# Performance work log

Measured on AMD Instinct MI355X. Metric: run time of the kernel, lower is better.

## Reference

```python
import jax, jax.numpy as jnp
import numpy as np

N = 100000
E = 1600000


def gcn_conv(x, W, b, src, dst, n_nodes):
    """PyG GCNConv: linear -> add self loops -> sym-normalized scatter-add."""
    h = x @ W  # [N, out]
    # degree with self-loops: deg[i] = 1 + in_degree(i)
    deg = jax.ops.segment_sum(jnp.ones((src.shape[0],), h.dtype), dst,
                              num_segments=n_nodes) + 1.0
    dinv = jax.lax.rsqrt(deg)  # deg >= 1 always
    norm = dinv[src] * dinv[dst]  # [E]
    # neighbor messages + self-loop contribution (norm = deg^-1)
    agg = jax.ops.segment_sum(h[src] * norm[:, None], dst,
                              num_segments=n_nodes)
    return agg + h * (dinv * dinv)[:, None] + b


def setup_inputs() -> dict:
    key = jax.random.key(0)
    k1, k2, k3, k4 = jax.random.split(key, 4)
    x = jax.random.normal(k1, (N, 128), dtype=jnp.float32)
    edge_index = jax.random.randint(k2, (2, E), 0, N, dtype=jnp.int64)
    W1 = jax.random.normal(k3, (128, 64), dtype=jnp.float32) * (1.0 / np.sqrt(128))
    b1 = jnp.zeros((64,), jnp.float32)
    W2 = jax.random.normal(k4, (64, 40), dtype=jnp.float32) * (1.0 / np.sqrt(64))
    b2 = jnp.zeros((40,), jnp.float32)
    return {"x": x, "edge_index": edge_index, "W1": W1, "b1": b1,
            "W2": W2, "b2": b2}


def reference(x, edge_index, W1, b1, W2, b2):
    src, dst = edge_index[0], edge_index[1]
    h = gcn_conv(x, W1, b1, src, dst, N)
    h = jax.nn.relu(h)
    # dropout is identity in eval mode; mask_features is a no-op
    h = gcn_conv(h, W2, b2, src, dst, N)
    return jax.nn.log_softmax(h, axis=1)
```

## Files before the change

### kernel.cpp

```cpp
#include <hip/hip_runtime.h>
#include <math.h>

#define N_NODES 100000
#define N_EDGES 1600000
#define F_IN    128
#define F_HID   64
#define F_OUT   40

#define BIN_SHIFT 9
#define NBINS     196
#define BIN_CAP   10240
#define FILL_BLOCKS 256

typedef unsigned int  uint;
typedef unsigned short ushort;
typedef __attribute__((ext_vector_type(8))) short bf16x8;
typedef __attribute__((ext_vector_type(4))) float f32x4;

__device__ __forceinline__ unsigned short f2bf(float f) {
    uint u = __float_as_uint(f);
    u = (u + 0x7FFF + ((u >> 16) & 1)) >> 16;
    return (unsigned short)u;
}
__device__ __forceinline__ uint pack2bf(float a, float b) {
    return (uint)f2bf(a) | ((uint)f2bf(b) << 16);
}
__device__ __forceinline__ float bf_lo(uint u) { return __uint_as_float(u << 16); }
__device__ __forceinline__ float bf_hi(uint u) { return __uint_as_float(u & 0xFFFF0000u); }

__global__ void init_kernel(int* __restrict__ bcursor) {
    int t = threadIdx.x;
    if (t < NBINS) bcursor[t] = t * BIN_CAP;
}

__global__ void binfill_kernel(const int* __restrict__ src, const int* __restrict__ dst,
                               int* __restrict__ bcursor, int* __restrict__ bins, int E) {
    __shared__ int lcount[NBINS];
    __shared__ int gbase[NBINS];
    int tid = threadIdx.x;
    for (int i = tid; i < NBINS; i += 256) lcount[i] = 0;
    __syncthreads();
    int chunk = (E + gridDim.x - 1) / gridDim.x;
    int beg = blockIdx.x * chunk, end = min(E, beg + chunk);
    for (int e = beg + tid; e < end; e += 256)
        atomicAdd(&lcount[dst[e] >> BIN_SHIFT], 1);
    __syncthreads();
    for (int i = tid; i < NBINS; i += 256) {
        gbase[i] = lcount[i] ? atomicAdd(&bcursor[i], lcount[i]) : 0;
        lcount[i] = 0;
    }
    __syncthreads();
    for (int e = beg + tid; e < end; e += 256) {
        int d = dst[e];
        int b = d >> BIN_SHIFT;
        int p = atomicAdd(&lcount[b], 1);
        bins[gbase[b] + p] = src[e] | ((d & 511) << 17);
    }
}

__global__ void binsort_kernel(const int* __restrict__ bcursor, const int* __restrict__ bins,
                               int* __restrict__ csr, int* __restrict__ rowstart,
                               int* __restrict__ rowcnt, float* __restrict__ dinv) {
    __shared__ int hist[512];
    __shared__ int scan[512];
    __shared__ int cur[512];
    __shared__ int sorted[BIN_CAP];
    int b = blockIdx.x, t = threadIdx.x;
    int base = b * BIN_CAP;
    int cnt = bcursor[b] - base;
    hist[t] = 0;
    __syncthreads();
    for (int i = t; i < cnt; i += 512)
        atomicAdd(&hist[(unsigned)bins[base + i] >> 17], 1);
    __syncthreads();
    int v = hist[t];
    scan[t] = v;
    __syncthreads();
    for (int off = 1; off < 512; off <<= 1) {
        int u = (t >= off) ? scan[t - off] : 0;
        __syncthreads();
        scan[t] += u;
        __syncthreads();
    }
    int excl = scan[t] - v;
    cur[t] = excl;
    int node = (b << BIN_SHIFT) + t;
    if (node < N_NODES) {
        rowstart[node] = base + excl;
        rowcnt[node]   = v;
        dinv[node] = rsqrtf((float)v + 1.0f);
    }
    __syncthreads();
    for (int i = t; i < cnt; i += 512) {
        int p   = bins[base + i];
        int pos = atomicAdd(&cur[(unsigned)p >> 17], 1);
        sorted[pos] = p & 0x1FFFF;
    }
    __syncthreads();
    for (int i = t; i < cnt; i += 512)
        csr[base + i] = sorted[i];
}

__global__ void wtrans_kernel(const float* __restrict__ W, uint* __restrict__ Wt) {
    int tid = threadIdx.x;
    for (int i = tid; i < 4096; i += 256) {
        int c  = i >> 6;
        int kp = i & 63;
        Wt[i] = pack2bf(W[(2 * kp) * F_HID + c], W[(2 * kp + 1) * F_HID + c]);
    }
}

#define XPITCH 68
__global__ __launch_bounds__(256) void gemm1_kernel(const float* __restrict__ x,
                                                    const uint* __restrict__ Wt,
                                                    ushort* __restrict__ h, int n) {
    __shared__ __align__(16) uint Xu[64 * XPITCH];
    __shared__ __align__(16) uint Wu[64 * XPITCH];
    int tid = threadIdx.x;
    int node0 = blockIdx.x * 64;

    {
        int c = tid >> 2, qq = tid & 3;
        const uint4* gsrc = (const uint4*)&Wt[c * 64 + qq * 16];
        uint4* ldst = (uint4*)&Wu[c * XPITCH + qq * 16];
        #pragma unroll
        for (int j = 0; j < 4; ++j) ldst[j] = gsrc[j];
    }
    {
        int row = tid >> 2, qq = tid & 3;
        int node = node0 + row;
        uint4* ldst = (uint4*)&Xu[row * XPITCH + qq * 16];
        if (node < n) {
            const float4* gsrc = (const float4*)&x[(size_t)node * F_IN + qq * 32];
            #pragma unroll
            for (int j = 0; j < 4; ++j) {
                float4 a = gsrc[2 * j], b = gsrc[2 * j + 1];
                uint4 o;
                o.x = pack2bf(a.x, a.y); o.y = pack2bf(a.z, a.w);
                o.z = pack2bf(b.x, b.y); o.w = pack2bf(b.z, b.w);
                ldst[j] = o;
            }
        } else {
            uint4 z = make_uint4(0, 0, 0, 0);
            #pragma unroll
            for (int j = 0; j < 4; ++j) ldst[j] = z;
        }
    }
    __syncthreads();

    int wv   = tid >> 6;
    int lane = tid & 63;
    int lrow = lane & 15;
    int quad = lane >> 4;

    bf16x8 bfrag[4][4];
    #pragma unroll
    for (int t = 0; t < 4; ++t)
        #pragma unroll
        for (int s = 0; s < 4; ++s)
            bfrag[t][s] = *(const bf16x8*)&Wu[(t * 16 + lrow) * XPITCH + s * 16 + quad * 4];

    f32x4 acc[4];
    #pragma unroll
    for (int t = 0; t < 4; ++t) acc[t] = (f32x4){0.f, 0.f, 0.f, 0.f};

    #pragma unroll
    for (int s = 0; s < 4; ++s) {
        bf16x8 afrag = *(const bf16x8*)&Xu[(wv * 16 + lrow) * XPITCH + s * 16 + quad * 4];
        #pragma unroll
        for (int t = 0; t < 4; ++t)
            acc[t] = __builtin_amdgcn_mfma_f32_16x16x32_bf16(afrag, bfrag[t][s], acc[t], 0, 0, 0);
    }

    #pragma unroll
    for (int t = 0; t < 4; ++t) {
        #pragma unroll
        for (int i = 0; i < 4; ++i) {
            int node = node0 + wv * 16 + quad * 4 + i;
            if (node < n) h[(size_t)node * F_HID + t * 16 + lrow] = f2bf(acc[t][i]);
        }
    }
}

__global__ void agg1_kernel(const int* __restrict__ rowstart, const int* __restrict__ rowcnt,
                            const int* __restrict__ csr, const float* __restrict__ dinv,
                            const ushort* __restrict__ h, const float* __restrict__ b,
                            ushort* __restrict__ out, int n) {
    int wv   = threadIdx.x >> 6;
    int lane = threadIdx.x & 63;
    int slot = lane >> 3;
    int c    = lane & 7;
    int node0 = blockIdx.x * 16 + wv * 4;
    for (int nn = 0; nn < 4; ++nn) {
        int node = node0 + nn;
        if (node >= n) break;
        int beg = rowstart[node], end = beg + rowcnt[node];
        float acc[8] = {0.f,0.f,0.f,0.f,0.f,0.f,0.f,0.f};
        for (int base = beg; base < end; base += 64) {
            int idx = base + lane;
            int   sid = 0; float wgt = 0.f;
            if (idx < end) { sid = csr[idx]; wgt = dinv[sid]; }
            int cnt    = min(64, end - base);
            int groups = (cnt + 7) >> 3;
            int g = 0;
            for (; g + 2 <= groups; g += 2) {
                int   sA = __shfl(sid, g * 8 + slot);
                float wA = __shfl(wgt, g * 8 + slot);
                int   sB = __shfl(sid, g * 8 + 8 + slot);
                float wB = __shfl(wgt, g * 8 + 8 + slot);
                uint4 hA = *(const uint4*)&h[(size_t)sA * F_HID + (c << 3)];
                uint4 hB = *(const uint4*)&h[(size_t)sB * F_HID + (c << 3)];
                acc[0] += bf_lo(hA.x) * wA; acc[1] += bf_hi(hA.x) * wA;
                acc[2] += bf_lo(hA.y) * wA; acc[3] += bf_hi(hA.y) * wA;
                acc[4] += bf_lo(hA.z) * wA; acc[5] += bf_hi(hA.z) * wA;
                acc[6] += bf_lo(hA.w) * wA; acc[7] += bf_hi(hA.w) * wA;
                acc[0] += bf_lo(hB.x) * wB; acc[1] += bf_hi(hB.x) * wB;
                acc[2] += bf_lo(hB.y) * wB; acc[3] += bf_hi(hB.y) * wB;
                acc[4] += bf_lo(hB.z) * wB; acc[5] += bf_hi(hB.z) * wB;
                acc[6] += bf_lo(hB.w) * wB; acc[7] += bf_hi(hB.w) * wB;
            }
            if (g < groups) {
                int   sA = __shfl(sid, g * 8 + slot);
                float wA = __shfl(wgt, g * 8 + slot);
                uint4 hA = *(const uint4*)&h[(size_t)sA * F_HID + (c << 3)];
                acc[0] += bf_lo(hA.x) * wA; acc[1] += bf_hi(hA.x) * wA;
                acc[2] += bf_lo(hA.y) * wA; acc[3] += bf_hi(hA.y) * wA;
                acc[4] += bf_lo(hA.z) * wA; acc[5] += bf_hi(hA.z) * wA;
                acc[6] += bf_lo(hA.w) * wA; acc[7] += bf_hi(hA.w) * wA;
            }
        }
        #pragma unroll
        for (int m = 8; m < 64; m <<= 1) {
            #pragma unroll
            for (int k = 0; k < 8; ++k) acc[k] += __shfl_xor(acc[k], m);
        }
        if (slot == 0) {
            float di = dinv[node];
            uint4 hs = *(const uint4*)&h[(size_t)node * F_HID + (c << 3)];
            float self[8] = { bf_lo(hs.x), bf_hi(hs.x), bf_lo(hs.y), bf_hi(hs.y),
                              bf_lo(hs.z), bf_hi(hs.z), bf_lo(hs.w), bf_hi(hs.w) };
            float4 b0 = *(const float4*)&b[c << 3];
            float4 b1v = *(const float4*)&b[(c << 3) + 4];
            float bb[8] = { b0.x, b0.y, b0.z, b0.w, b1v.x, b1v.y, b1v.z, b1v.w };
            ushort o[8];
            #pragma unroll
            for (int k = 0; k < 8; ++k) {
                float v = fmaxf(acc[k] * di + self[k] * di * di + bb[k], 0.f);
                o[k] = f2bf(v);
            }
            uint4 pk;
            pk.x = (uint)o[0] | ((uint)o[1] << 16);
            pk.y = (uint)o[2] | ((uint)o[3] << 16);
            pk.z = (uint)o[4] | ((uint)o[5] << 16);
            pk.w = (uint)o[6] | ((uint)o[7] << 16);
            *(uint4*)&out[(size_t)node * F_HID + (c << 3)] = pk;
        }
    }
}

__global__ void gemm2_kernel(const ushort* __restrict__ a, const float* __restrict__ W,
                             ushort* __restrict__ h, int n) {
    __shared__ float Wl[F_HID * F_OUT];
    int tid = threadIdx.x;
    for (int i = tid; i < F_HID * F_OUT; i += 256) Wl[i] = W[i];
    __syncthreads();
    long long idx = (long long)blockIdx.x * 256 + tid;
    if (idx >= (long long)n * F_OUT) return;
    int node = (int)(idx / F_OUT);
    int col  = (int)(idx - (long long)node * F_OUT);
    const uint* arow = (const uint*)(a + (size_t)node * F_HID);
    float acc = 0.0f;
    #pragma unroll 8
    for (int k = 0; k < F_HID / 2; ++k) {
        uint u = arow[k];
        acc += bf_lo(u) * Wl[(2 * k) * F_OUT + col] + bf_hi(u) * Wl[(2 * k + 1) * F_OUT + col];
    }
    h[idx] = f2bf(acc);
}

__global__ void agg2_kernel(const int* __restrict__ rowstart, const int* __restrict__ rowcnt,
                            const int* __restrict__ csr, const float* __restrict__ dinv,
                            const ushort* __restrict__ h, const float* __restrict__ b,
                            float* __restrict__ out, int n) {
    int wv   = threadIdx.x >> 6;
    int lane = threadIdx.x & 63;
    int slot = lane / 5;
    int c    = lane - slot * 5;
    int node0 = blockIdx.x * 16 + wv * 4;
    float bb[8];
    if (lane < 5) {
        float4 b0 = *(const float4*)&b[lane * 8];
        float4 b1 = *(const float4*)&b[lane * 8 + 4];
        bb[0] = b0.x; bb[1] = b0.y; bb[2] = b0.z; bb[3] = b0.w;
        bb[4] = b1.x; bb[5] = b1.y; bb[6] = b1.z; bb[7] = b1.w;
    }
    for (int nn = 0; nn < 4; ++nn) {
        int node = node0 + nn;
        if (node >= n) break;
        int beg = rowstart[node], end = beg + rowcnt[node];
        float acc[8] = {0.f,0.f,0.f,0.f,0.f,0.f,0.f,0.f};
        for (int base = beg; base < end; base += 60) {
            int idx = base + lane;
            int   sid = 0; float wgt = 0.f;
            if (lane < 60 && idx < end) { sid = csr[idx]; wgt = dinv[sid]; }
            int cnt    = min(60, end - base);
            int groups = (cnt + 11) / 12;
            int g = 0;
            for (; g + 2 <= groups; g += 2) {
                int   slA = (slot < 12) ? (g * 12 + slot) : 60;
                int   slB = (slot < 12) ? (g * 12 + 12 + slot) : 60;
                int   sA = __shfl(sid, slA);
                float wA = __shfl(wgt, slA);
                int   sB = __shfl(sid, slB);
                float wB = __shfl(wgt, slB);
                uint4 hA = *(const uint4*)&h[(size_t)sA * F_OUT + c * 8];
                uint4 hB = *(const uint4*)&h[(size_t)sB * F_OUT + c * 8];
                acc[0] += bf_lo(hA.x) * wA; acc[1] += bf_hi(hA.x) * wA;
                acc[2] += bf_lo(hA.y) * wA; acc[3] += bf_hi(hA.y) * wA;
                acc[4] += bf_lo(hA.z) * wA; acc[5] += bf_hi(hA.z) * wA;
                acc[6] += bf_lo(hA.w) * wA; acc[7] += bf_hi(hA.w) * wA;
                acc[0] += bf_lo(hB.x) * wB; acc[1] += bf_hi(hB.x) * wB;
                acc[2] += bf_lo(hB.y) * wB; acc[3] += bf_hi(hB.y) * wB;
                acc[4] += bf_lo(hB.z) * wB; acc[5] += bf_hi(hB.z) * wB;
                acc[6] += bf_lo(hB.w) * wB; acc[7] += bf_hi(hB.w) * wB;
            }
            if (g < groups) {
                int   slA = (slot < 12) ? (g * 12 + slot) : 60;
                int   sA = __shfl(sid, slA);
                float wA = __shfl(wgt, slA);
                uint4 hA = *(const uint4*)&h[(size_t)sA * F_OUT + c * 8];
                acc[0] += bf_lo(hA.x) * wA; acc[1] += bf_hi(hA.x) * wA;
                acc[2] += bf_lo(hA.y) * wA; acc[3] += bf_hi(hA.y) * wA;
                acc[4] += bf_lo(hA.z) * wA; acc[5] += bf_hi(hA.z) * wA;
                acc[6] += bf_lo(hA.w) * wA; acc[7] += bf_hi(hA.w) * wA;
            }
        }
        float r[8];
        #pragma unroll
        for (int k = 0; k < 8; ++k) {
            float t6 = __shfl(acc[k], lane + 30);
            float s6 = acc[k] + t6;
            float t3 = __shfl(s6, lane + 15);
            float s3 = s6 + t3;
            float t1 = __shfl(s3, lane + 5);
            float t2 = __shfl(s3, lane + 10);
            r[k] = s3 + t1 + t2;
        }
        float val[8];
        float m = -INFINITY;
        if (lane < 5) {
            float di = dinv[node];
            uint4 hs = *(const uint4*)&h[(size_t)node * F_OUT + lane * 8];
            float self[8] = { bf_lo(hs.x), bf_hi(hs.x), bf_lo(hs.y), bf_hi(hs.y),
                              bf_lo(hs.z), bf_hi(hs.z), bf_lo(hs.w), bf_hi(hs.w) };
            #pragma unroll
            for (int k = 0; k < 8; ++k) {
                val[k] = r[k] * di + self[k] * di * di + bb[k];
                m = fmaxf(m, val[k]);
            }
        }
        #pragma unroll
        for (int off = 1; off < 8; off <<= 1) m = fmaxf(m, __shfl_xor(m, off));
        float p = 0.f;
        if (lane < 5) {
            #pragma unroll
            for (int k = 0; k < 8; ++k) p += __expf(val[k] - m);
        }
        #pragma unroll
        for (int off = 1; off < 8; off <<= 1) p += __shfl_xor(p, off);
        float lse = m + __logf(p);
        if (lane < 5) {
            float4 o0, o1;
            o0.x = val[0] - lse; o0.y = val[1] - lse; o0.z = val[2] - lse; o0.w = val[3] - lse;
            o1.x = val[4] - lse; o1.y = val[5] - lse; o1.z = val[6] - lse; o1.w = val[7] - lse;
            *(float4*)&out[(size_t)node * F_OUT + lane * 8]     = o0;
            *(float4*)&out[(size_t)node * F_OUT + lane * 8 + 4] = o1;
        }
    }
}

extern "C" void kernel_launch(void* const* d_in, const int* in_sizes, int n_in,
                              void* d_out, int out_size, void* d_ws, size_t ws_size,
                              hipStream_t stream) {
    const float* x  = (const float*)d_in[0];
    const int*   ei = (const int*)d_in[1];
    const float* W1 = (const float*)d_in[2];
    const float* b1 = (const float*)d_in[3];
    const float* W2 = (const float*)d_in[4];
    const float* b2 = (const float*)d_in[5];
    const int* src = ei;
    const int* dst = ei + N_EDGES;

    char* p = (char*)d_ws;
    int*    bcursor  = (int*)p;     p += (size_t)(NBINS + 4) * 4;
    int*    bins     = (int*)p;     p += (size_t)NBINS * BIN_CAP * 4;
    int*    csr_src  = (int*)p;     p += (size_t)NBINS * BIN_CAP * 4;
    int*    rowstart = (int*)p;     p += (size_t)(N_NODES + 4) * 4;
    int*    rowcnt   = (int*)p;     p += (size_t)(N_NODES + 4) * 4;
    float*  dinv     = (float*)p;   p += (size_t)N_NODES * 4;
    uint*   Wtb      = (uint*)p;    p += (size_t)4096 * 4;
    ushort* h1b      = (ushort*)p;  p += (size_t)N_NODES * F_HID * 2;
    ushort* out1b    = (ushort*)p;  p += (size_t)N_NODES * F_HID * 2;
    ushort* h2b      = (ushort*)p;  p += (size_t)N_NODES * F_OUT * 2;
    float*  out      = (float*)d_out;

    init_kernel   <<<1, 256, 0, stream>>>(bcursor);
    binfill_kernel<<<FILL_BLOCKS, 256, 0, stream>>>(src, dst, bcursor, bins, N_EDGES);
    binsort_kernel<<<NBINS, 512, 0, stream>>>(bcursor, bins, csr_src, rowstart, rowcnt, dinv);
    wtrans_kernel <<<1, 256, 0, stream>>>(W1, Wtb);
    gemm1_kernel  <<<(N_NODES + 63) / 64, 256, 0, stream>>>(x, Wtb, h1b, N_NODES);
    agg1_kernel   <<<(N_NODES + 15) / 16, 256, 0, stream>>>(rowstart, rowcnt, csr_src, dinv,
                                                            h1b, b1, out1b, N_NODES);
    gemm2_kernel  <<<((N_NODES * F_OUT) + 255) / 256, 256, 0, stream>>>(out1b, W2, h2b, N_NODES);
    agg2_kernel   <<<(N_NODES + 15) / 16, 256, 0, stream>>>(rowstart, rowcnt, csr_src, dinv,
                                                            h2b, b2, out, N_NODES);
}
```

Baseline: 303.0 us.

## Halve bin size, fuse prep kernels, one node per wavefront in aggregation

```diff
diff --git a/kernel.cpp b/kernel.cpp
--- a/kernel.cpp
+++ b/kernel.cpp
@@ -7,10 +7,10 @@
 #define F_HID   64
 #define F_OUT   40
 
-#define BIN_SHIFT 9
-#define NBINS     196
-#define BIN_CAP   10240
-#define FILL_BLOCKS 256
+#define BIN_SHIFT 8
+#define NBINS     392
+#define BIN_CAP   5120
+#define FILL_BLOCKS 512
 
 typedef unsigned int  uint;
 typedef unsigned short ushort;
@@ -28,9 +28,15 @@
 __device__ __forceinline__ float bf_lo(uint u) { return __uint_as_float(u << 16); }
 __device__ __forceinline__ float bf_hi(uint u) { return __uint_as_float(u & 0xFFFF0000u); }
 
-__global__ void init_kernel(int* __restrict__ bcursor) {
-    int t = threadIdx.x;
-    if (t < NBINS) bcursor[t] = t * BIN_CAP;
+__global__ void prep_kernel(const float* __restrict__ W, uint* __restrict__ Wt,
+                            int* __restrict__ bcursor) {
+    int tid = threadIdx.x;
+    if (tid < NBINS) bcursor[tid] = tid * BIN_CAP;
+    for (int i = tid; i < 4096; i += 512) {
+        int c  = i >> 6;
+        int kp = i & 63;
+        Wt[i] = pack2bf(W[(2 * kp) * F_HID + c], W[(2 * kp + 1) * F_HID + c]);
+    }
 }
 
 __global__ void binfill_kernel(const int* __restrict__ src, const int* __restrict__ dst,
@@ -54,41 +60,43 @@
         int d = dst[e];
         int b = d >> BIN_SHIFT;
         int p = atomicAdd(&lcount[b], 1);
-        bins[gbase[b] + p] = src[e] | ((d & 511) << 17);
+        bins[gbase[b] + p] = src[e] | ((d & 255) << 17);
     }
 }
 
 __global__ void binsort_kernel(const int* __restrict__ bcursor, const int* __restrict__ bins,
                                int* __restrict__ csr, int* __restrict__ rowstart,
                                int* __restrict__ rowcnt, float* __restrict__ dinv) {
-    __shared__ int hist[512];
-    __shared__ int scan[512];
-    __shared__ int cur[512];
+    __shared__ int hist[256];
+    __shared__ int scan[256];
+    __shared__ int cur[256];
     __shared__ int sorted[BIN_CAP];
     int b = blockIdx.x, t = threadIdx.x;
     int base = b * BIN_CAP;
     int cnt = bcursor[b] - base;
-    hist[t] = 0;
+    if (t < 256) hist[t] = 0;
     __syncthreads();
     for (int i = t; i < cnt; i += 512)
         atomicAdd(&hist[(unsigned)bins[base + i] >> 17], 1);
     __syncthreads();
-    int v = hist[t];
-    scan[t] = v;
-    __syncthreads();
-    for (int off = 1; off < 512; off <<= 1) {
-        int u = (t >= off) ? scan[t - off] : 0;
+    int v = 0;
+    if (t < 256) { v = hist[t]; scan[t] = v; }
+    __syncthreads();
+    for (int off = 1; off < 256; off <<= 1) {
+        int u = (t < 256 && t >= off) ? scan[t - off] : 0;
         __syncthreads();
-        scan[t] += u;
+        if (t < 256) scan[t] += u;
         __syncthreads();
     }
-    int excl = scan[t] - v;
-    cur[t] = excl;
-    int node = (b << BIN_SHIFT) + t;
-    if (node < N_NODES) {
-        rowstart[node] = base + excl;
-        rowcnt[node]   = v;
-        dinv[node] = rsqrtf((float)v + 1.0f);
+    if (t < 256) {
+        int excl = scan[t] - v;
+        cur[t] = excl;
+        int node = (b << BIN_SHIFT) + t;
+        if (node < N_NODES) {
+            rowstart[node] = base + excl;
+            rowcnt[node]   = v;
+            dinv[node] = rsqrtf((float)v + 1.0f);
+        }
     }
     __syncthreads();
     for (int i = t; i < cnt; i += 512) {
@@ -99,15 +107,6 @@
     __syncthreads();
     for (int i = t; i < cnt; i += 512)
         csr[base + i] = sorted[i];
-}
-
-__global__ void wtrans_kernel(const float* __restrict__ W, uint* __restrict__ Wt) {
-    int tid = threadIdx.x;
-    for (int i = tid; i < 4096; i += 256) {
-        int c  = i >> 6;
-        int kp = i & 63;
-        Wt[i] = pack2bf(W[(2 * kp) * F_HID + c], W[(2 * kp + 1) * F_HID + c]);
-    }
 }
 
 #define XPITCH 68
@@ -186,75 +185,71 @@
                             const int* __restrict__ csr, const float* __restrict__ dinv,
                             const ushort* __restrict__ h, const float* __restrict__ b,
                             ushort* __restrict__ out, int n) {
-    int wv   = threadIdx.x >> 6;
+    int node = blockIdx.x * 4 + (threadIdx.x >> 6);
     int lane = threadIdx.x & 63;
+    if (node >= n) return;
     int slot = lane >> 3;
     int c    = lane & 7;
-    int node0 = blockIdx.x * 16 + wv * 4;
-    for (int nn = 0; nn < 4; ++nn) {
-        int node = node0 + nn;
-        if (node >= n) break;
-        int beg = rowstart[node], end = beg + rowcnt[node];
-        float acc[8] = {0.f,0.f,0.f,0.f,0.f,0.f,0.f,0.f};
-        for (int base = beg; base < end; base += 64) {
-            int idx = base + lane;
-            int   sid = 0; float wgt = 0.f;
-            if (idx < end) { sid = csr[idx]; wgt = dinv[sid]; }
-            int cnt    = min(64, end - base);
-            int groups = (cnt + 7) >> 3;
-            int g = 0;
-            for (; g + 2 <= groups; g += 2) {
-                int   sA = __shfl(sid, g * 8 + slot);
-                float wA = __shfl(wgt, g * 8 + slot);
-                int   sB = __shfl(sid, g * 8 + 8 + slot);
-                float wB = __shfl(wgt, g * 8 + 8 + slot);
-                uint4 hA = *(const uint4*)&h[(size_t)sA * F_HID + (c << 3)];
-                uint4 hB = *(const uint4*)&h[(size_t)sB * F_HID + (c << 3)];
-                acc[0] += bf_lo(hA.x) * wA; acc[1] += bf_hi(hA.x) * wA;
-                acc[2] += bf_lo(hA.y) * wA; acc[3] += bf_hi(hA.y) * wA;
-                acc[4] += bf_lo(hA.z) * wA; acc[5] += bf_hi(hA.z) * wA;
-                acc[6] += bf_lo(hA.w) * wA; acc[7] += bf_hi(hA.w) * wA;
-                acc[0] += bf_lo(hB.x) * wB; acc[1] += bf_hi(hB.x) * wB;
-                acc[2] += bf_lo(hB.y) * wB; acc[3] += bf_hi(hB.y) * wB;
-                acc[4] += bf_lo(hB.z) * wB; acc[5] += bf_hi(hB.z) * wB;
-                acc[6] += bf_lo(hB.w) * wB; acc[7] += bf_hi(hB.w) * wB;
-            }
-            if (g < groups) {
-                int   sA = __shfl(sid, g * 8 + slot);
-                float wA = __shfl(wgt, g * 8 + slot);
-                uint4 hA = *(const uint4*)&h[(size_t)sA * F_HID + (c << 3)];
-                acc[0] += bf_lo(hA.x) * wA; acc[1] += bf_hi(hA.x) * wA;
-                acc[2] += bf_lo(hA.y) * wA; acc[3] += bf_hi(hA.y) * wA;
-                acc[4] += bf_lo(hA.z) * wA; acc[5] += bf_hi(hA.z) * wA;
-                acc[6] += bf_lo(hA.w) * wA; acc[7] += bf_hi(hA.w) * wA;
-            }
-        }
-        #pragma unroll
-        for (int m = 8; m < 64; m <<= 1) {
-            #pragma unroll
-            for (int k = 0; k < 8; ++k) acc[k] += __shfl_xor(acc[k], m);
-        }
-        if (slot == 0) {
-            float di = dinv[node];
-            uint4 hs = *(const uint4*)&h[(size_t)node * F_HID + (c << 3)];
-            float self[8] = { bf_lo(hs.x), bf_hi(hs.x), bf_lo(hs.y), bf_hi(hs.y),
-                              bf_lo(hs.z), bf_hi(hs.z), bf_lo(hs.w), bf_hi(hs.w) };
-            float4 b0 = *(const float4*)&b[c << 3];
-            float4 b1v = *(const float4*)&b[(c << 3) + 4];
-            float bb[8] = { b0.x, b0.y, b0.z, b0.w, b1v.x, b1v.y, b1v.z, b1v.w };
-            ushort o[8];
-            #pragma unroll
-            for (int k = 0; k < 8; ++k) {
-                float v = fmaxf(acc[k] * di + self[k] * di * di + bb[k], 0.f);
-                o[k] = f2bf(v);
-            }
-            uint4 pk;
-            pk.x = (uint)o[0] | ((uint)o[1] << 16);
-            pk.y = (uint)o[2] | ((uint)o[3] << 16);
-            pk.z = (uint)o[4] | ((uint)o[5] << 16);
-            pk.w = (uint)o[6] | ((uint)o[7] << 16);
-            *(uint4*)&out[(size_t)node * F_HID + (c << 3)] = pk;
-        }
+    int beg = rowstart[node], end = beg + rowcnt[node];
+    float acc[8] = {0.f,0.f,0.f,0.f,0.f,0.f,0.f,0.f};
+    for (int base = beg; base < end; base += 64) {
+        int idx = base + lane;
+        int   sid = 0; float wgt = 0.f;
+        if (idx < end) { sid = csr[idx]; wgt = dinv[sid]; }
+        int cnt    = min(64, end - base);
+        int groups = (cnt + 7) >> 3;
+        int g = 0;
+        for (; g + 2 <= groups; g += 2) {
+            int   sA = __shfl(sid, g * 8 + slot);
+            float wA = __shfl(wgt, g * 8 + slot);
+            int   sB = __shfl(sid, g * 8 + 8 + slot);
+            float wB = __shfl(wgt, g * 8 + 8 + slot);
+            uint4 hA = *(const uint4*)&h[(size_t)sA * F_HID + (c << 3)];
+            uint4 hB = *(const uint4*)&h[(size_t)sB * F_HID + (c << 3)];
+            acc[0] += bf_lo(hA.x) * wA; acc[1] += bf_hi(hA.x) * wA;
+            acc[2] += bf_lo(hA.y) * wA; acc[3] += bf_hi(hA.y) * wA;
+            acc[4] += bf_lo(hA.z) * wA; acc[5] += bf_hi(hA.z) * wA;
+            acc[6] += bf_lo(hA.w) * wA; acc[7] += bf_hi(hA.w) * wA;
+            acc[0] += bf_lo(hB.x) * wB; acc[1] += bf_hi(hB.x) * wB;
+            acc[2] += bf_lo(hB.y) * wB; acc[3] += bf_hi(hB.y) * wB;
+            acc[4] += bf_lo(hB.z) * wB; acc[5] += bf_hi(hB.z) * wB;
+            acc[6] += bf_lo(hB.w) * wB; acc[7] += bf_hi(hB.w) * wB;
+        }
+        if (g < groups) {
+            int   sA = __shfl(sid, g * 8 + slot);
+            float wA = __shfl(wgt, g * 8 + slot);
+            uint4 hA = *(const uint4*)&h[(size_t)sA * F_HID + (c << 3)];
+            acc[0] += bf_lo(hA.x) * wA; acc[1] += bf_hi(hA.x) * wA;
+            acc[2] += bf_lo(hA.y) * wA; acc[3] += bf_hi(hA.y) * wA;
+            acc[4] += bf_lo(hA.z) * wA; acc[5] += bf_hi(hA.z) * wA;
+            acc[6] += bf_lo(hA.w) * wA; acc[7] += bf_hi(hA.w) * wA;
+        }
+    }
+    #pragma unroll
+    for (int m = 8; m < 64; m <<= 1) {
+        #pragma unroll
+        for (int k = 0; k < 8; ++k) acc[k] += __shfl_xor(acc[k], m);
+    }
+    if (slot == 0) {
+        float di = dinv[node];
+        uint4 hs = *(const uint4*)&h[(size_t)node * F_HID + (c << 3)];
+        float self[8] = { bf_lo(hs.x), bf_hi(hs.x), bf_lo(hs.y), bf_hi(hs.y),
+                          bf_lo(hs.z), bf_hi(hs.z), bf_lo(hs.w), bf_hi(hs.w) };
+        float4 b0 = *(const float4*)&b[c << 3];
+        float4 b1v = *(const float4*)&b[(c << 3) + 4];
+        float bb[8] = { b0.x, b0.y, b0.z, b0.w, b1v.x, b1v.y, b1v.z, b1v.w };
+        ushort o[8];
+        #pragma unroll
+        for (int k = 0; k < 8; ++k) {
+            float v = fmaxf(acc[k] * di + self[k] * di * di + bb[k], 0.f);
+            o[k] = f2bf(v);
+        }
+        uint4 pk;
+        pk.x = (uint)o[0] | ((uint)o[1] << 16);
+        pk.y = (uint)o[2] | ((uint)o[3] << 16);
+        pk.z = (uint)o[4] | ((uint)o[5] << 16);
+        pk.w = (uint)o[6] | ((uint)o[7] << 16);
+        *(uint4*)&out[(size_t)node * F_HID + (c << 3)] = pk;
     }
 }
 
@@ -282,11 +277,11 @@
                             const int* __restrict__ csr, const float* __restrict__ dinv,
                             const ushort* __restrict__ h, const float* __restrict__ b,
                             float* __restrict__ out, int n) {
-    int wv   = threadIdx.x >> 6;
+    int node = blockIdx.x * 4 + (threadIdx.x >> 6);
     int lane = threadIdx.x & 63;
+    if (node >= n) return;
     int slot = lane / 5;
     int c    = lane - slot * 5;
-    int node0 = blockIdx.x * 16 + wv * 4;
     float bb[8];
     if (lane < 5) {
         float4 b0 = *(const float4*)&b[lane * 8];
@@ -294,88 +289,84 @@
         bb[0] = b0.x; bb[1] = b0.y; bb[2] = b0.z; bb[3] = b0.w;
         bb[4] = b1.x; bb[5] = b1.y; bb[6] = b1.z; bb[7] = b1.w;
     }
-    for (int nn = 0; nn < 4; ++nn) {
-        int node = node0 + nn;
-        if (node >= n) break;
-        int beg = rowstart[node], end = beg + rowcnt[node];
-        float acc[8] = {0.f,0.f,0.f,0.f,0.f,0.f,0.f,0.f};
-        for (int base = beg; base < end; base += 60) {
-            int idx = base + lane;
-            int   sid = 0; float wgt = 0.f;
-            if (lane < 60 && idx < end) { sid = csr[idx]; wgt = dinv[sid]; }
-            int cnt    = min(60, end - base);
-            int groups = (cnt + 11) / 12;
-            int g = 0;
-            for (; g + 2 <= groups; g += 2) {
-                int   slA = (slot < 12) ? (g * 12 + slot) : 60;
-                int   slB = (slot < 12) ? (g * 12 + 12 + slot) : 60;
-                int   sA = __shfl(sid, slA);
-                float wA = __shfl(wgt, slA);
-                int   sB = __shfl(sid, slB);
-                float wB = __shfl(wgt, slB);
-                uint4 hA = *(const uint4*)&h[(size_t)sA * F_OUT + c * 8];
-                uint4 hB = *(const uint4*)&h[(size_t)sB * F_OUT + c * 8];
-                acc[0] += bf_lo(hA.x) * wA; acc[1] += bf_hi(hA.x) * wA;
-                acc[2] += bf_lo(hA.y) * wA; acc[3] += bf_hi(hA.y) * wA;
-                acc[4] += bf_lo(hA.z) * wA; acc[5] += bf_hi(hA.z) * wA;
-                acc[6] += bf_lo(hA.w) * wA; acc[7] += bf_hi(hA.w) * wA;
-                acc[0] += bf_lo(hB.x) * wB; acc[1] += bf_hi(hB.x) * wB;
-                acc[2] += bf_lo(hB.y) * wB; acc[3] += bf_hi(hB.y) * wB;
-                acc[4] += bf_lo(hB.z) * wB; acc[5] += bf_hi(hB.z) * wB;
-                acc[6] += bf_lo(hB.w) * wB; acc[7] += bf_hi(hB.w) * wB;
-            }
-            if (g < groups) {
-                int   slA = (slot < 12) ? (g * 12 + slot) : 60;
-                int   sA = __shfl(sid, slA);
-                float wA = __shfl(wgt, slA);
-                uint4 hA = *(const uint4*)&h[(size_t)sA * F_OUT + c * 8];
-                acc[0] += bf_lo(hA.x) * wA; acc[1] += bf_hi(hA.x) * wA;
-                acc[2] += bf_lo(hA.y) * wA; acc[3] += bf_hi(hA.y) * wA;
-                acc[4] += bf_lo(hA.z) * wA; acc[5] += bf_hi(hA.z) * wA;
-                acc[6] += bf_lo(hA.w) * wA; acc[7] += bf_hi(hA.w) * wA;
-            }
-        }
-        float r[8];
+    int beg = rowstart[node], end = beg + rowcnt[node];
+    float acc[8] = {0.f,0.f,0.f,0.f,0.f,0.f,0.f,0.f};
+    for (int base = beg; base < end; base += 60) {
+        int idx = base + lane;
+        int   sid = 0; float wgt = 0.f;
+        if (lane < 60 && idx < end) { sid = csr[idx]; wgt = dinv[sid]; }
+        int cnt    = min(60, end - base);
+        int groups = (cnt + 11) / 12;
+        int g = 0;
+        for (; g + 2 <= groups; g += 2) {
+            int   slA = (slot < 12) ? (g * 12 + slot) : 60;
+            int   slB = (slot < 12) ? (g * 12 + 12 + slot) : 60;
+            int   sA = __shfl(sid, slA);
+            float wA = __shfl(wgt, slA);
+            int   sB = __shfl(sid, slB);
+            float wB = __shfl(wgt, slB);
+            uint4 hA = *(const uint4*)&h[(size_t)sA * F_OUT + c * 8];
+            uint4 hB = *(const uint4*)&h[(size_t)sB * F_OUT + c * 8];
+            acc[0] += bf_lo(hA.x) * wA; acc[1] += bf_hi(hA.x) * wA;
+            acc[2] += bf_lo(hA.y) * wA; acc[3] += bf_hi(hA.y) * wA;
+            acc[4] += bf_lo(hA.z) * wA; acc[5] += bf_hi(hA.z) * wA;
+            acc[6] += bf_lo(hA.w) * wA; acc[7] += bf_hi(hA.w) * wA;
+            acc[0] += bf_lo(hB.x) * wB; acc[1] += bf_hi(hB.x) * wB;
+            acc[2] += bf_lo(hB.y) * wB; acc[3] += bf_hi(hB.y) * wB;
+            acc[4] += bf_lo(hB.z) * wB; acc[5] += bf_hi(hB.z) * wB;
+            acc[6] += bf_lo(hB.w) * wB; acc[7] += bf_hi(hB.w) * wB;
+        }
+        if (g < groups) {
+            int   slA = (slot < 12) ? (g * 12 + slot) : 60;
+            int   sA = __shfl(sid, slA);
+            float wA = __shfl(wgt, slA);
+            uint4 hA = *(const uint4*)&h[(size_t)sA * F_OUT + c * 8];
+            acc[0] += bf_lo(hA.x) * wA; acc[1] += bf_hi(hA.x) * wA;
+            acc[2] += bf_lo(hA.y) * wA; acc[3] += bf_hi(hA.y) * wA;
+            acc[4] += bf_lo(hA.z) * wA; acc[5] += bf_hi(hA.z) * wA;
+            acc[6] += bf_lo(hA.w) * wA; acc[7] += bf_hi(hA.w) * wA;
+        }
+    }
+    float r[8];
+    #pragma unroll
+    for (int k = 0; k < 8; ++k) {
+        float t6 = __shfl(acc[k], lane + 30);
+        float s6 = acc[k] + t6;
+        float t3 = __shfl(s6, lane + 15);
+        float s3 = s6 + t3;
+        float t1 = __shfl(s3, lane + 5);
+        float t2 = __shfl(s3, lane + 10);
+        r[k] = s3 + t1 + t2;
+    }
+    float val[8];
+    float m = -INFINITY;
+    if (lane < 5) {
+        float di = dinv[node];
+        uint4 hs = *(const uint4*)&h[(size_t)node * F_OUT + lane * 8];
+        float self[8] = { bf_lo(hs.x), bf_hi(hs.x), bf_lo(hs.y), bf_hi(hs.y),
+                          bf_lo(hs.z), bf_hi(hs.z), bf_lo(hs.w), bf_hi(hs.w) };
         #pragma unroll
         for (int k = 0; k < 8; ++k) {
-            float t6 = __shfl(acc[k], lane + 30);
-            float s6 = acc[k] + t6;
-            float t3 = __shfl(s6, lane + 15);
-            float s3 = s6 + t3;
-            float t1 = __shfl(s3, lane + 5);
-            float t2 = __shfl(s3, lane + 10);
-            r[k] = s3 + t1 + t2;
-        }
-        float val[8];
-        float m = -INFINITY;
-        if (lane < 5) {
-            float di = dinv[node];
-            uint4 hs = *(const uint4*)&h[(size_t)node * F_OUT + lane * 8];
-            float self[8] = { bf_lo(hs.x), bf_hi(hs.x), bf_lo(hs.y), bf_hi(hs.y),
-                              bf_lo(hs.z), bf_hi(hs.z), bf_lo(hs.w), bf_hi(hs.w) };
-            #pragma unroll
-            for (int k = 0; k < 8; ++k) {
-                val[k] = r[k] * di + self[k] * di * di + bb[k];
-                m = fmaxf(m, val[k]);
-            }
-        }
-        #pragma unroll
-        for (int off = 1; off < 8; off <<= 1) m = fmaxf(m, __shfl_xor(m, off));
-        float p = 0.f;
-        if (lane < 5) {
-            #pragma unroll
-            for (int k = 0; k < 8; ++k) p += __expf(val[k] - m);
-        }
-        #pragma unroll
-        for (int off = 1; off < 8; off <<= 1) p += __shfl_xor(p, off);
-        float lse = m + __logf(p);
-        if (lane < 5) {
-            float4 o0, o1;
-            o0.x = val[0] - lse; o0.y = val[1] - lse; o0.z = val[2] - lse; o0.w = val[3] - lse;
-            o1.x = val[4] - lse; o1.y = val[5] - lse; o1.z = val[6] - lse; o1.w = val[7] - lse;
-            *(float4*)&out[(size_t)node * F_OUT + lane * 8]     = o0;
-            *(float4*)&out[(size_t)node * F_OUT + lane * 8 + 4] = o1;
-        }
+            val[k] = r[k] * di + self[k] * di * di + bb[k];
+            m = fmaxf(m, val[k]);
+        }
+    }
+    #pragma unroll
+    for (int off = 1; off < 8; off <<= 1) m = fmaxf(m, __shfl_xor(m, off));
+    float p = 0.f;
+    if (lane < 5) {
+        #pragma unroll
+        for (int k = 0; k < 8; ++k) p += __expf(val[k] - m);
+    }
+    #pragma unroll
+    for (int off = 1; off < 8; off <<= 1) p += __shfl_xor(p, off);
+    float lse = m + __logf(p);
+    if (lane < 5) {
+        float4 o0, o1;
+        o0.x = val[0] - lse; o0.y = val[1] - lse; o0.z = val[2] - lse; o0.w = val[3] - lse;
+        o1.x = val[4] - lse; o1.y = val[5] - lse; o1.z = val[6] - lse; o1.w = val[7] - lse;
+        *(float4*)&out[(size_t)node * F_OUT + lane * 8]     = o0;
+        *(float4*)&out[(size_t)node * F_OUT + lane * 8 + 4] = o1;
     }
 }
 
@@ -392,7 +383,7 @@
     const int* dst = ei + N_EDGES;
 
     char* p = (char*)d_ws;
-    int*    bcursor  = (int*)p;     p += (size_t)(NBINS + 4) * 4;
+    int*    bcursor  = (int*)p;     p += (size_t)(NBINS + 8) * 4;
     int*    bins     = (int*)p;     p += (size_t)NBINS * BIN_CAP * 4;
     int*    csr_src  = (int*)p;     p += (size_t)NBINS * BIN_CAP * 4;
     int*    rowstart = (int*)p;     p += (size_t)(N_NODES + 4) * 4;
@@ -404,14 +395,13 @@
     ushort* h2b      = (ushort*)p;  p += (size_t)N_NODES * F_OUT * 2;
     float*  out      = (float*)d_out;
 
-    init_kernel   <<<1, 256, 0, stream>>>(bcursor);
+    prep_kernel   <<<1, 512, 0, stream>>>(W1, Wtb, bcursor);
     binfill_kernel<<<FILL_BLOCKS, 256, 0, stream>>>(src, dst, bcursor, bins, N_EDGES);
     binsort_kernel<<<NBINS, 512, 0, stream>>>(bcursor, bins, csr_src, rowstart, rowcnt, dinv);
-    wtrans_kernel <<<1, 256, 0, stream>>>(W1, Wtb);
     gemm1_kernel  <<<(N_NODES + 63) / 64, 256, 0, stream>>>(x, Wtb, h1b, N_NODES);
-    agg1_kernel   <<<(N_NODES + 15) / 16, 256, 0, stream>>>(rowstart, rowcnt, csr_src, dinv,
-                                                            h1b, b1, out1b, N_NODES);
+    agg1_kernel   <<<(N_NODES + 3) / 4, 256, 0, stream>>>(rowstart, rowcnt, csr_src, dinv,
+                                                          h1b, b1, out1b, N_NODES);
     gemm2_kernel  <<<((N_NODES * F_OUT) + 255) / 256, 256, 0, stream>>>(out1b, W2, h2b, N_NODES);
-    agg2_kernel   <<<(N_NODES + 15) / 16, 256, 0, stream>>>(rowstart, rowcnt, csr_src, dinv,
-                                                            h2b, b2, out, N_NODES);
-}
+    agg2_kernel   <<<(N_NODES + 3) / 4, 256, 0, stream>>>(rowstart, rowcnt, csr_src, dinv,
+                                                          h2b, b2, out, N_NODES);
+}
```

Measured after the change: 288.2 us. 1.05x faster.
